# Kernel tuning notes

Measured on AMD Instinct MI355X. Metric: run time of the kernel, lower is better.

The kernel has to match this reference:

```python
import jax, jax.numpy as jnp
import numpy as np

D_IN = 768      # encoder feature dim (hardcoded in GRUCell(768, d_model))
D_MODEL = 256   # hidden size
B, T = 64, 512


def _gru_cell(x, h, W_ih, W_hh, b_ih, b_hh):
    # PyTorch GRUCell math. W_ih: [in, 3H], W_hh: [H, 3H], biases [3H].
    gi = x @ W_ih + b_ih
    gh = h @ W_hh + b_hh
    i_r, i_z, i_n = jnp.split(gi, 3, axis=-1)
    h_r, h_z, h_n = jnp.split(gh, 3, axis=-1)
    r = jax.nn.sigmoid(i_r + h_r)
    z = jax.nn.sigmoid(i_z + h_z)
    n = jnp.tanh(i_n + r * h_n)
    return (1.0 - z) * n + z * h


def setup_inputs() -> dict:
    key = jax.random.key(0)
    ks = jax.random.split(key, 10)
    s_in = 1.0 / np.sqrt(D_MODEL)
    inp = {
        "encoder_outputs": jax.random.normal(ks[0], (B, T, D_IN), jnp.float32),
        "tau1": jnp.array([1.0], jnp.float32),
        "tau2": jnp.array([1.2], jnp.float32),
        "W_ih1": jax.random.normal(ks[1], (D_IN, 3 * D_MODEL), jnp.float32) * s_in,
        "W_hh1": jax.random.normal(ks[2], (D_MODEL, 3 * D_MODEL), jnp.float32) * s_in,
        "b_ih1": jax.random.normal(ks[3], (3 * D_MODEL,), jnp.float32) * s_in,
        "b_hh1": jax.random.normal(ks[4], (3 * D_MODEL,), jnp.float32) * s_in,
        "W_ih2": jax.random.normal(ks[5], (D_IN + D_MODEL, 3 * D_MODEL), jnp.float32) * s_in,
        "W_hh2": jax.random.normal(ks[6], (D_MODEL, 3 * D_MODEL), jnp.float32) * s_in,
        "b_ih2": jax.random.normal(ks[7], (3 * D_MODEL,), jnp.float32) * s_in,
        "b_hh2": jax.random.normal(ks[8], (3 * D_MODEL,), jnp.float32) * s_in,
    }
    return inp


def reference(encoder_outputs, tau1, tau2, W_ih1, W_hh1, b_ih1, b_hh1,
              W_ih2, W_hh2, b_ih2, b_hh2):
    bsz = encoder_outputs.shape[0]
    inv_t1 = 1.0 / tau1  # [1], broadcasts over [B, H]
    inv_t2 = 1.0 / tau2
    h0 = (jnp.zeros((bsz, D_MODEL), encoder_outputs.dtype),
          jnp.zeros((bsz, D_MODEL), encoder_outputs.dtype))

    xs = jnp.swapaxes(encoder_outputs, 0, 1)  # [T, B, D_IN]

    def step(carry, x_t):
        h1, h2 = carry
        h1_ = _gru_cell(x_t, h1, W_ih1, W_hh1, b_ih1, b_hh1)
        h1 = (1.0 - inv_t1) * h1 + inv_t1 * h1_
        x2 = jnp.concatenate([x_t, h1], axis=1)
        h2_ = _gru_cell(x2, h2, W_ih2, W_hh2, b_ih2, b_hh2)
        h2 = (1.0 - inv_t2) * h2 + inv_t2 * h2_
        return (h1, h2), (h1, h2)

    _, (o1, o2) = jax.lax.scan(step, h0, xs)  # each [T, B, H]
    out = jnp.concatenate([o1, o2], axis=2)   # [T, B, 2H]
    out = jnp.swapaxes(out, 0, 1)             # [B, T, 2H]
    # Note: F.dropout(p=0.5) in the original is stochastic; omitted here
    # (identity) so the reference is deterministic for kernel comparison.
    return out
```

## Files before the change

kernel.cpp:

```cpp
#include <hip/hip_runtime.h>

typedef _Float16 f16;
typedef _Float16 f16x2 __attribute__((ext_vector_type(2)));
typedef _Float16 f16x8 __attribute__((ext_vector_type(8)));
typedef float f32x4 __attribute__((ext_vector_type(4)));
typedef unsigned int u32;
typedef unsigned short u16;

#define B_SZ 64
#define T_SZ 512
#define DIN 768
#define H_SZ 256
#define TH 768
#define M_ROWS (B_SZ * T_SZ)

#define O_WT1 ((size_t)0)
#define O_WT2 (O_WT1 + (size_t)768 * 768 * 2)
#define O_H1 (O_WT2 + (size_t)768 * 1024 * 2)
#define O_G (O_H1 + (size_t)M_ROWS * H_SZ * 2)

__device__ __forceinline__ u32 pk2(float a, float b) {
  union { f16 h[2]; u32 u; } x;
  x.h[0] = (f16)a;
  x.h[1] = (f16)b;
  return x.u;
}

__device__ __forceinline__ float dot2f(u32 w, u32 h, float acc) {
#if __has_builtin(__builtin_amdgcn_fdot2)
  union { u32 u; f16x2 v; } a, b;
  a.u = w;
  b.u = h;
  return __builtin_amdgcn_fdot2(a.v, b.v, acc, false);
#else
  union { u32 u; f16 h[2]; } a, b;
  a.u = w;
  b.u = h;
  acc = fmaf((float)a.h[0], (float)b.h[0], acc);
  acc = fmaf((float)a.h[1], (float)b.h[1], acc);
  return acc;
#endif
}

__device__ __forceinline__ float sigmf_(float x) {
  return 1.0f / (1.0f + __expf(-x));
}
__device__ __forceinline__ float tanhf_(float x) {
  float e = __expf(-2.0f * fabsf(x));
  float r = (1.0f - e) / (1.0f + e);
  return copysignf(r, x);
}

__global__ __launch_bounds__(256) void k_transpose(const float* __restrict__ W,
                                                   f16* __restrict__ Wt, int K,
                                                   int N) {
  __shared__ f16 tile[32][33];
  int tx = threadIdx.x, ty = threadIdx.y;
  int n0 = blockIdx.x * 32, k0 = blockIdx.y * 32;
#pragma unroll
  for (int q = 0; q < 4; ++q) {
    int k = k0 + ty + q * 8;
    tile[ty + q * 8][tx] = (f16)W[(size_t)k * N + n0 + tx];
  }
  __syncthreads();
#pragma unroll
  for (int q = 0; q < 4; ++q) {
    int n = n0 + ty + q * 8;
    Wt[(size_t)n * K + k0 + tx] = tile[tx][ty + q * 8];
  }
}

#define LDK 40
__global__ __launch_bounds__(256, 2) void k_gemm(
    const float* __restrict__ A32, const f16* __restrict__ AH,
    const f16* __restrict__ Bt, const float* __restrict__ bias,
    f16* __restrict__ C, int K, int bstride) {
  __shared__ __align__(16) f16 Asm[128 * LDK];
  __shared__ __align__(16) f16 Bsm[128 * LDK];
  int tid = threadIdx.x;
  int lane = tid & 63, wave = tid >> 6;
  int wm = wave & 1, wn = wave >> 1;
  int fm = lane & 15, fk = (lane >> 4) * 8;
  int srow = tid >> 1, skp = (tid & 1) * 16;
  size_t r0 = (size_t)blockIdx.y * 128;
  int n0 = blockIdx.x * 128;
  f32x4 acc[4][4] = {};

  for (int k0 = 0; k0 < K; k0 += 32) {
    __syncthreads();
    if (k0 < DIN) {
      const float* src = A32 + (r0 + srow) * DIN + k0 + skp;
      float4 v0 = *(const float4*)(src);
      float4 v1 = *(const float4*)(src + 4);
      float4 v2 = *(const float4*)(src + 8);
      float4 v3 = *(const float4*)(src + 12);
      uint4 w0 = make_uint4(pk2(v0.x, v0.y), pk2(v0.z, v0.w), pk2(v1.x, v1.y),
                            pk2(v1.z, v1.w));
      uint4 w1 = make_uint4(pk2(v2.x, v2.y), pk2(v2.z, v2.w), pk2(v3.x, v3.y),
                            pk2(v3.z, v3.w));
      *(uint4*)&Asm[srow * LDK + skp] = w0;
      *(uint4*)&Asm[srow * LDK + skp + 8] = w1;
    } else {
      const uint4* src =
          (const uint4*)(AH + (r0 + srow) * H_SZ + (k0 - DIN) + skp);
      *(uint4*)&Asm[srow * LDK + skp] = src[0];
      *(uint4*)&Asm[srow * LDK + skp + 8] = src[1];
    }
    const uint4* bsrc =
        (const uint4*)(Bt + (size_t)(n0 + srow) * bstride + k0 + skp);
    *(uint4*)&Bsm[srow * LDK + skp] = bsrc[0];
    *(uint4*)&Bsm[srow * LDK + skp + 8] = bsrc[1];
    __syncthreads();

    f16x8 af[4], bf[4];
#pragma unroll
    for (int mt = 0; mt < 4; ++mt)
      af[mt] = *(const f16x8*)&Asm[(wm * 64 + mt * 16 + fm) * LDK + fk];
#pragma unroll
    for (int nt = 0; nt < 4; ++nt)
      bf[nt] = *(const f16x8*)&Bsm[(wn * 64 + nt * 16 + fm) * LDK + fk];
#pragma unroll
    for (int mt = 0; mt < 4; ++mt)
#pragma unroll
      for (int nt = 0; nt < 4; ++nt)
        acc[mt][nt] = __builtin_amdgcn_mfma_f32_16x16x32_f16(af[mt], bf[nt],
                                                             acc[mt][nt], 0, 0, 0);
  }

  int ccol = lane & 15, crb = (lane >> 4) * 4;
#pragma unroll
  for (int nt = 0; nt < 4; ++nt) {
    int col = n0 + wn * 64 + nt * 16 + ccol;
    float bv = bias[col];
#pragma unroll
    for (int mt = 0; mt < 4; ++mt) {
      size_t rb = r0 + wm * 64 + mt * 16 + crb;
#pragma unroll
      for (int rg = 0; rg < 4; ++rg)
        C[(rb + rg) * TH + col] = (f16)(acc[mt][nt][rg] + bv);
    }
  }
}

__global__ __launch_bounds__(512, 2) void k_rec(
    const f16* __restrict__ G, const float* __restrict__ Whh,
    const float* __restrict__ bhh, const float* __restrict__ tau,
    float* __restrict__ out, int out_off, f16* __restrict__ H1out) {
  __shared__ __align__(16) u16 s_h16[256];
  __shared__ float s_h32[256];
  __shared__ float s_part[256 * 3];
  __shared__ __align__(16) f16 s_stage[32 * TH];

  int tid = threadIdx.x;
  int b = blockIdx.x;
  int cg = tid & 255;
  int kh = tid >> 8;

  u32 w2[3][64];
#pragma unroll
  for (int ch = 0; ch < 8; ++ch) {
    int kc = ch * 32;
    __syncthreads();
#pragma unroll
    for (int q = 0; q < 12; ++q) {
      int idx4 = tid + q * 512;
      float4 v = *(const float4*)(Whh + (size_t)kc * TH + (size_t)idx4 * 4);
      union { f16 h[4]; uint2 u; } pw;
      pw.h[0] = (f16)v.x;
      pw.h[1] = (f16)v.y;
      pw.h[2] = (f16)v.z;
      pw.h[3] = (f16)v.w;
      *(uint2*)&s_stage[idx4 * 4] = pw.u;
    }
    __syncthreads();
    if ((kc >> 7) == kh) {
      int ib = (kc & 127) >> 1;
#pragma unroll
      for (int i2 = 0; i2 < 16; ++i2) {
#pragma unroll
        for (int c = 0; c < 3; ++c) {
          int col = cg + c * 256;
          w2[c][ib + i2] = pk2((float)s_stage[(2 * i2) * TH + col],
                               (float)s_stage[(2 * i2 + 1) * TH + col]);
        }
      }
    }
  }

  float bb0 = bhh[cg], bb1 = bhh[cg + 256], bb2 = bhh[cg + 512];
  float invt = 1.0f / tau[0];
  float om = 1.0f - invt;
  if (tid < 256) {
    s_h16[tid] = 0;
    s_h32[tid] = 0.0f;
  }
  __syncthreads();

  const f16* gbase = G + (size_t)b * T_SZ * TH;
  float* obase = out + (size_t)b * T_SZ * 512 + out_off;
  f16* hbase = H1out ? H1out + (size_t)b * T_SZ * H_SZ : (f16*)0;
  const uint4* hv4 = (const uint4*)s_h16 + kh * 16;

  for (int t = 0; t < T_SZ; ++t) {
    f16 gg0 = (f16)0.f, gg1 = (f16)0.f, gg2 = (f16)0.f;
    if (tid < 256) {
      const f16* gp = gbase + (size_t)t * TH + cg;
      gg0 = gp[0];
      gg1 = gp[256];
      gg2 = gp[512];
    }
    float a0 = 0.f, a1 = 0.f, a2 = 0.f;
#pragma unroll
    for (int ii = 0; ii < 16; ++ii) {
      uint4 hv = hv4[ii];
      a0 = dot2f(w2[0][ii * 4 + 0], hv.x, a0);
      a1 = dot2f(w2[1][ii * 4 + 0], hv.x, a1);
      a2 = dot2f(w2[2][ii * 4 + 0], hv.x, a2);
      a0 = dot2f(w2[0][ii * 4 + 1], hv.y, a0);
      a1 = dot2f(w2[1][ii * 4 + 1], hv.y, a1);
      a2 = dot2f(w2[2][ii * 4 + 1], hv.y, a2);
      a0 = dot2f(w2[0][ii * 4 + 2], hv.z, a0);
      a1 = dot2f(w2[1][ii * 4 + 2], hv.z, a1);
      a2 = dot2f(w2[2][ii * 4 + 2], hv.z, a2);
      a0 = dot2f(w2[0][ii * 4 + 3], hv.w, a0);
      a1 = dot2f(w2[1][ii * 4 + 3], hv.w, a1);
      a2 = dot2f(w2[2][ii * 4 + 3], hv.w, a2);
    }
    if (kh) {
      s_part[cg * 3 + 0] = a0;
      s_part[cg * 3 + 1] = a1;
      s_part[cg * 3 + 2] = a2;
    }
    __syncthreads();
    if (tid < 256) {
      float ghr = a0 + s_part[cg * 3 + 0] + bb0;
      float ghz = a1 + s_part[cg * 3 + 1] + bb1;
      float ghn = a2 + s_part[cg * 3 + 2] + bb2;
      float r = sigmf_((float)gg0 + ghr);
      float z = sigmf_((float)gg1 + ghz);
      float n = tanhf_((float)gg2 + r * ghn);
      float hold = s_h32[cg];
      float hc = (1.0f - z) * n + z * hold;
      float hn2 = om * hold + invt * hc;
      s_h32[cg] = hn2;
      union { f16 h; u16 s; } hb;
      hb.h = (f16)hn2;
      s_h16[cg] = hb.s;
      obase[(size_t)t * 512 + cg] = hn2;
      if (hbase) hbase[(size_t)t * H_SZ + cg] = (f16)hn2;
    }
    __syncthreads();
  }
}

extern "C" void kernel_launch(void* const* d_in, const int* in_sizes, int n_in,
                              void* d_out, int out_size, void* d_ws,
                              size_t ws_size, hipStream_t stream) {
  const float* enc = (const float*)d_in[0];
  const float* tau1 = (const float*)d_in[1];
  const float* tau2 = (const float*)d_in[2];
  const float* Wih1 = (const float*)d_in[3];
  const float* Whh1 = (const float*)d_in[4];
  const float* bih1 = (const float*)d_in[5];
  const float* bhh1 = (const float*)d_in[6];
  const float* Wih2 = (const float*)d_in[7];
  const float* Whh2 = (const float*)d_in[8];
  const float* bih2 = (const float*)d_in[9];
  const float* bhh2 = (const float*)d_in[10];
  float* out = (float*)d_out;
  char* ws = (char*)d_ws;

  f16* Wt1 = (f16*)(ws + O_WT1);
  f16* Wt2 = (f16*)(ws + O_WT2);
  f16* H1 = (f16*)(ws + O_H1);
  f16* G = (f16*)(ws + O_G);

  k_transpose<<<dim3(24, 24), dim3(32, 8), 0, stream>>>(Wih1, Wt1, 768, 768);
  k_transpose<<<dim3(24, 32), dim3(32, 8), 0, stream>>>(Wih2, Wt2, 1024, 768);

  k_gemm<<<dim3(6, 256), 256, 0, stream>>>(enc, (const f16*)0, Wt1, bih1, G,
                                           768, 768);
  k_rec<<<64, 512, 0, stream>>>(G, Whh1, bhh1, tau1, out, 0, H1);

  k_gemm<<<dim3(6, 256), 256, 0, stream>>>(enc, H1, Wt2, bih2, G, 1024, 1024);
  k_rec<<<64, 512, 0, stream>>>(G, Whh2, bhh2, tau2, out, 256, (f16*)0);
}
```

Measured before the change: 1.520 ms.

## Double-buffer hidden state, prefetch gate inputs, keep weights in vector registers

Rewrites the recurrent kernel. The fp32 hidden state now lives in a register instead of shared memory, and the fp16 hidden vector is double-buffered in shared memory. The input-gate values for the next timestep are prefetched while the current step is computed, so global load latency is hidden behind the dot products. Weights are loaded straight from global memory into ext_vector registers, which removes the shared-memory staging and its barriers, and the cross-half partial sums are exchanged as a single float4. It keeps the same two barriers per step but carries the same heavy register load.

```diff
diff --git a/kernel.cpp b/kernel.cpp
--- a/kernel.cpp
+++ b/kernel.cpp
@@ -6,6 +6,7 @@
 typedef float f32x4 __attribute__((ext_vector_type(4)));
 typedef unsigned int u32;
 typedef unsigned short u16;
+typedef u32 u32x32 __attribute__((ext_vector_type(32)));
 
 #define B_SZ 64
 #define T_SZ 512
@@ -146,109 +147,121 @@
     const f16* __restrict__ G, const float* __restrict__ Whh,
     const float* __restrict__ bhh, const float* __restrict__ tau,
     float* __restrict__ out, int out_off, f16* __restrict__ H1out) {
-  __shared__ __align__(16) u16 s_h16[256];
-  __shared__ float s_h32[256];
-  __shared__ float s_part[256 * 3];
-  __shared__ __align__(16) f16 s_stage[32 * TH];
-
-  int tid = threadIdx.x;
-  int b = blockIdx.x;
-  int cg = tid & 255;
-  int kh = tid >> 8;
-
-  u32 w2[3][64];
-#pragma unroll
-  for (int ch = 0; ch < 8; ++ch) {
-    int kc = ch * 32;
+  __shared__ __align__(16) u16 s_h16[2][256];
+  __shared__ __align__(16) float4 s_part[256];
+
+  const int tid = threadIdx.x;
+  const int b = blockIdx.x;
+  const int cg = tid & 255;
+  const int kh = tid >> 8;
+
+  u32x32 w0a, w0b, w1a, w1b, w2a, w2b;
+  {
+    const float* base = Whh + (size_t)(kh * 128) * TH + cg;
+#pragma unroll
+    for (int j = 0; j < 32; ++j) {
+      const float* p = base + (size_t)(2 * j) * TH;
+      w0a[j] = pk2(p[0], p[TH]);
+      w1a[j] = pk2(p[256], p[TH + 256]);
+      w2a[j] = pk2(p[512], p[TH + 512]);
+    }
+#pragma unroll
+    for (int j = 0; j < 32; ++j) {
+      const float* p = base + (size_t)(64 + 2 * j) * TH;
+      w0b[j] = pk2(p[0], p[TH]);
+      w1b[j] = pk2(p[256], p[TH + 256]);
+      w2b[j] = pk2(p[512], p[TH + 512]);
+    }
+  }
+
+  const float bb0 = bhh[cg], bb1 = bhh[cg + 256], bb2 = bhh[cg + 512];
+  const float invt = 1.0f / tau[0];
+  const float om = 1.0f - invt;
+
+  if (tid < 256) s_h16[0][cg] = 0;
+
+  const f16* gbase = G + (size_t)b * T_SZ * TH + cg;
+  float* obase = out + (size_t)b * T_SZ * 512 + out_off + cg;
+  f16* hbase = H1out ? H1out + (size_t)b * T_SZ * H_SZ + cg : (f16*)0;
+
+  float hreg = 0.0f;
+  f16 g0 = (f16)0.f, g1 = (f16)0.f, g2 = (f16)0.f;
+  if (tid < 256) {
+    g0 = gbase[0];
+    g1 = gbase[256];
+    g2 = gbase[512];
+  }
+  __syncthreads();
+
+  for (int t = 0; t < T_SZ; ++t) {
+    f16 n0 = (f16)0.f, n1 = (f16)0.f, n2 = (f16)0.f;
+    {
+      const int tn = (t + 1 < T_SZ) ? t + 1 : t;
+      if (tid < 256) {
+        const f16* gp = gbase + (size_t)tn * TH;
+        n0 = gp[0];
+        n1 = gp[256];
+        n2 = gp[512];
+      }
+    }
+
+    const uint4* hv4 = (const uint4*)(&s_h16[t & 1][0]) + kh * 16;
+    float a0 = 0.f, a1 = 0.f, a2 = 0.f;
+#pragma unroll
+    for (int ii = 0; ii < 8; ++ii) {
+      uint4 hv = hv4[ii];
+      a0 = dot2f(w0a[4 * ii + 0], hv.x, a0);
+      a1 = dot2f(w1a[4 * ii + 0], hv.x, a1);
+      a2 = dot2f(w2a[4 * ii + 0], hv.x, a2);
+      a0 = dot2f(w0a[4 * ii + 1], hv.y, a0);
+      a1 = dot2f(w1a[4 * ii + 1], hv.y, a1);
+      a2 = dot2f(w2a[4 * ii + 1], hv.y, a2);
+      a0 = dot2f(w0a[4 * ii + 2], hv.z, a0);
+      a1 = dot2f(w1a[4 * ii + 2], hv.z, a1);
+      a2 = dot2f(w2a[4 * ii + 2], hv.z, a2);
+      a0 = dot2f(w0a[4 * ii + 3], hv.w, a0);
+      a1 = dot2f(w1a[4 * ii + 3], hv.w, a1);
+      a2 = dot2f(w2a[4 * ii + 3], hv.w, a2);
+    }
+#pragma unroll
+    for (int ii = 0; ii < 8; ++ii) {
+      uint4 hv = hv4[8 + ii];
+      a0 = dot2f(w0b[4 * ii + 0], hv.x, a0);
+      a1 = dot2f(w1b[4 * ii + 0], hv.x, a1);
+      a2 = dot2f(w2b[4 * ii + 0], hv.x, a2);
+      a0 = dot2f(w0b[4 * ii + 1], hv.y, a0);
+      a1 = dot2f(w1b[4 * ii + 1], hv.y, a1);
+      a2 = dot2f(w2b[4 * ii + 1], hv.y, a2);
+      a0 = dot2f(w0b[4 * ii + 2], hv.z, a0);
+      a1 = dot2f(w1b[4 * ii + 2], hv.z, a1);
+      a2 = dot2f(w2b[4 * ii + 2], hv.z, a2);
+      a0 = dot2f(w0b[4 * ii + 3], hv.w, a0);
+      a1 = dot2f(w1b[4 * ii + 3], hv.w, a1);
+      a2 = dot2f(w2b[4 * ii + 3], hv.w, a2);
+    }
+
+    if (kh) s_part[cg] = make_float4(a0, a1, a2, 0.f);
     __syncthreads();
-#pragma unroll
-    for (int q = 0; q < 12; ++q) {
-      int idx4 = tid + q * 512;
-      float4 v = *(const float4*)(Whh + (size_t)kc * TH + (size_t)idx4 * 4);
-      union { f16 h[4]; uint2 u; } pw;
-      pw.h[0] = (f16)v.x;
-      pw.h[1] = (f16)v.y;
-      pw.h[2] = (f16)v.z;
-      pw.h[3] = (f16)v.w;
-      *(uint2*)&s_stage[idx4 * 4] = pw.u;
-    }
-    __syncthreads();
-    if ((kc >> 7) == kh) {
-      int ib = (kc & 127) >> 1;
-#pragma unroll
-      for (int i2 = 0; i2 < 16; ++i2) {
-#pragma unroll
-        for (int c = 0; c < 3; ++c) {
-          int col = cg + c * 256;
-          w2[c][ib + i2] = pk2((float)s_stage[(2 * i2) * TH + col],
-                               (float)s_stage[(2 * i2 + 1) * TH + col]);
-        }
-      }
-    }
-  }
-
-  float bb0 = bhh[cg], bb1 = bhh[cg + 256], bb2 = bhh[cg + 512];
-  float invt = 1.0f / tau[0];
-  float om = 1.0f - invt;
-  if (tid < 256) {
-    s_h16[tid] = 0;
-    s_h32[tid] = 0.0f;
-  }
-  __syncthreads();
-
-  const f16* gbase = G + (size_t)b * T_SZ * TH;
-  float* obase = out + (size_t)b * T_SZ * 512 + out_off;
-  f16* hbase = H1out ? H1out + (size_t)b * T_SZ * H_SZ : (f16*)0;
-  const uint4* hv4 = (const uint4*)s_h16 + kh * 16;
-
-  for (int t = 0; t < T_SZ; ++t) {
-    f16 gg0 = (f16)0.f, gg1 = (f16)0.f, gg2 = (f16)0.f;
+
     if (tid < 256) {
-      const f16* gp = gbase + (size_t)t * TH + cg;
-      gg0 = gp[0];
-      gg1 = gp[256];
-      gg2 = gp[512];
-    }
-    float a0 = 0.f, a1 = 0.f, a2 = 0.f;
-#pragma unroll
-    for (int ii = 0; ii < 16; ++ii) {
-      uint4 hv = hv4[ii];
-      a0 = dot2f(w2[0][ii * 4 + 0], hv.x, a0);
-      a1 = dot2f(w2[1][ii * 4 + 0], hv.x, a1);
-      a2 = dot2f(w2[2][ii * 4 + 0], hv.x, a2);
-      a0 = dot2f(w2[0][ii * 4 + 1], hv.y, a0);
-      a1 = dot2f(w2[1][ii * 4 + 1], hv.y, a1);
-      a2 = dot2f(w2[2][ii * 4 + 1], hv.y, a2);
-      a0 = dot2f(w2[0][ii * 4 + 2], hv.z, a0);
-      a1 = dot2f(w2[1][ii * 4 + 2], hv.z, a1);
-      a2 = dot2f(w2[2][ii * 4 + 2], hv.z, a2);
-      a0 = dot2f(w2[0][ii * 4 + 3], hv.w, a0);
-      a1 = dot2f(w2[1][ii * 4 + 3], hv.w, a1);
-      a2 = dot2f(w2[2][ii * 4 + 3], hv.w, a2);
-    }
-    if (kh) {
-      s_part[cg * 3 + 0] = a0;
-      s_part[cg * 3 + 1] = a1;
-      s_part[cg * 3 + 2] = a2;
-    }
-    __syncthreads();
-    if (tid < 256) {
-      float ghr = a0 + s_part[cg * 3 + 0] + bb0;
-      float ghz = a1 + s_part[cg * 3 + 1] + bb1;
-      float ghn = a2 + s_part[cg * 3 + 2] + bb2;
-      float r = sigmf_((float)gg0 + ghr);
-      float z = sigmf_((float)gg1 + ghz);
-      float n = tanhf_((float)gg2 + r * ghn);
-      float hold = s_h32[cg];
-      float hc = (1.0f - z) * n + z * hold;
-      float hn2 = om * hold + invt * hc;
-      s_h32[cg] = hn2;
+      float4 pr = s_part[cg];
+      float ghr = a0 + pr.x + bb0;
+      float ghz = a1 + pr.y + bb1;
+      float ghn = a2 + pr.z + bb2;
+      float r = sigmf_((float)g0 + ghr);
+      float z = sigmf_((float)g1 + ghz);
+      float n = tanhf_((float)g2 + r * ghn);
+      float hc = (1.0f - z) * n + z * hreg;
+      hreg = om * hreg + invt * hc;
       union { f16 h; u16 s; } hb;
-      hb.h = (f16)hn2;
-      s_h16[cg] = hb.s;
-      obase[(size_t)t * 512 + cg] = hn2;
-      if (hbase) hbase[(size_t)t * H_SZ + cg] = (f16)hn2;
-    }
+      hb.h = (f16)hreg;
+      s_h16[(t + 1) & 1][cg] = hb.s;
+      obase[(size_t)t * 512] = hreg;
+      if (hbase) hbase[(size_t)t * H_SZ] = (f16)hreg;
+    }
+    g0 = n0;
+    g1 = n1;
+    g2 = n2;
     __syncthreads();
   }
 }
```

Measured after the change: 1.744 ms. 1.15x slower.
